# Kernel tuning notes

Hardware: AMD Instinct MI355X
Metric: run time of the kernel (lower is better)

Reference implementation:

```python
import jax, jax.numpy as jnp
import numpy as np

N_VARS = 28
HID = 64
BATCH = 32768
BN_EPS = 1e-5


def _lin_init(key, fan_in, shape):
    bound = 1.0 / np.sqrt(fan_in)
    return jax.random.uniform(key, shape, minval=-bound, maxval=bound, dtype=jnp.float32)


def setup_inputs() -> dict:
    key = jax.random.key(0)
    ks = jax.random.split(key, 8)
    n, h = N_VARS, HID
    X = jax.random.normal(ks[0], (BATCH, n), dtype=jnp.float32)
    W_logits = jax.random.uniform(ks[1], (n, n), minval=-0.01, maxval=0.01, dtype=jnp.float32)
    # per-mechanism (grouped) weights, stacked on leading mechanism axis n
    W1 = _lin_init(ks[2], n, (n, h, n)); b1 = _lin_init(ks[3], n, (n, h))
    W2 = _lin_init(ks[4], h, (n, h, h)); b2 = _lin_init(ks[5], h, (n, h))
    W3 = _lin_init(ks[6], h, (n, 1, h)); b3 = _lin_init(ks[7], h, (n, 1))
    gamma1 = jnp.ones((n, h)); beta1 = jnp.zeros((n, h))
    gamma2 = jnp.ones((n, h)); beta2 = jnp.zeros((n, h))
    return {"X": X, "W_logits": W_logits,
            "W1": W1, "b1": b1, "gamma1": gamma1, "beta1": beta1,
            "W2": W2, "b2": b2, "gamma2": gamma2, "beta2": beta2,
            "W3": W3, "b3": b3}


def _bn(x, gamma, beta):
    # x: [n, B, h]; batch stats over B (training-mode BatchNorm1d, biased var)
    m = x.mean(axis=1, keepdims=True)
    v = ((x - m) ** 2).mean(axis=1, keepdims=True)
    return gamma[:, None, :] * (x - m) * jax.lax.rsqrt(v + BN_EPS) + beta[:, None, :]


def reference(X, W_logits, W1, b1, gamma1, beta1, W2, b2, gamma2, beta2, W3, b3):
    n = W_logits.shape[0]
    # adjacency: sigmoid with zeroed diagonal
    W = jax.nn.sigmoid(W_logits) * (1.0 - jnp.eye(n, dtype=W_logits.dtype))
    # fuse the parent mask into the first layer's weights: one grouped GEMM
    # instead of n_vars separate masked matmuls
    W1_eff = W1 * W[:, None, :]                               # [n, h, n]
    h1 = jnp.einsum('bd,nhd->nbh', X, W1_eff) + b1[:, None, :]  # [n, B, h]
    a1 = jax.nn.gelu(_bn(h1, gamma1, beta1), approximate=False)
    h2 = jnp.einsum('nbh,ngh->nbg', a1, W2) + b2[:, None, :]
    a2 = jax.nn.gelu(_bn(h2, gamma2, beta2), approximate=False)
    out = jnp.einsum('nbh,noh->nbo', a2, W3) + b3[:, None, :]   # [n, B, 1]
    X_hat = out[:, :, 0].T                                     # [B, n]
    return (X_hat, W)
```

## Files before the change

### kernel.cpp

```cpp
#include <hip/hip_runtime.h>
#include <hip/hip_bf16.h>
#include <math.h>

typedef float  f4 __attribute__((ext_vector_type(4)));
typedef short  s8 __attribute__((ext_vector_type(8)));
typedef short  s4 __attribute__((ext_vector_type(4)));

#define NV 28
#define NB 32768
#define BN_EPS 1e-5f
#define NSLOT 434

#define SUM2_OFF   0
#define SSQ2_OFF   1792
#define BIAS1_OFF  3584
#define REDU_OFF   5376
#define PART_OFF   5824
#define BF_BASE_F  116992
#define W2B_OFF_S  57344
#define XBF_OFF_S  172032
#define H2_BYTE_OFF 2909184ull
#define H2_BYTES    117440512ull

__device__ __forceinline__ float gelu_f(float x) {
    float x2 = x * x;
    float z  = x * __builtin_fmaf(x2, -0.10294324f, -2.3022082f);
    float t  = __builtin_amdgcn_exp2f(z);
    return x * __builtin_amdgcn_rcpf(1.0f + t);
}
__device__ __forceinline__ unsigned short f2bf(float x) {
    unsigned u = __builtin_bit_cast(unsigned, x);
    return (unsigned short)((u + 0x7fffu + ((u >> 16) & 1u)) >> 16);
}
__device__ __forceinline__ float bf2f(short s) {
    return __builtin_bit_cast(float, ((int)(unsigned short)s) << 16);
}
__device__ __forceinline__ float row16_sum(float v) {
    int x;
    x = __builtin_amdgcn_update_dpp(0, __builtin_bit_cast(int, v), 0xB1, 0xF, 0xF, true);
    v += __builtin_bit_cast(float, x);
    x = __builtin_amdgcn_update_dpp(0, __builtin_bit_cast(int, v), 0x4E, 0xF, 0xF, true);
    v += __builtin_bit_cast(float, x);
    x = __builtin_amdgcn_update_dpp(0, __builtin_bit_cast(int, v), 0x124, 0xF, 0xF, true);
    v += __builtin_bit_cast(float, x);
    x = __builtin_amdgcn_update_dpp(0, __builtin_bit_cast(int, v), 0x128, 0xF, 0xF, true);
    v += __builtin_bit_cast(float, x);
    return v;
}
__device__ __forceinline__ float quad4_sum(float v) {
    int x;
    x = __builtin_amdgcn_update_dpp(0, __builtin_bit_cast(int, v), 0xB1, 0xF, 0xF, true);
    v += __builtin_bit_cast(float, x);
    x = __builtin_amdgcn_update_dpp(0, __builtin_bit_cast(int, v), 0x4E, 0xF, 0xF, true);
    v += __builtin_bit_cast(float, x);
    return v;
}

__global__ __launch_bounds__(256) void k_xstats(const float* __restrict__ X,
                                                float* __restrict__ ws) {
    __shared__ float sx[128 * 28];
    const int tid = threadIdx.x;
    const int rowbase = blockIdx.x * 128;
    {
        const f4* src = (const f4*)(X + (size_t)rowbase * 28);
        f4* dst = (f4*)sx;
        for (int i = tid; i < 128 * 28 / 4; i += 256) dst[i] = src[i];
    }
    __syncthreads();
    int* xb = (int*)((short*)(ws + BF_BASE_F) + XBF_OFF_S);
    for (int j = tid; j < 128 * 16; j += 256) {
        int row = j >> 4, cc = j & 15;
        float lo = (2 * cc     < 28) ? sx[row * 28 + 2 * cc]     : 0.0f;
        float hi = (2 * cc + 1 < 28) ? sx[row * 28 + 2 * cc + 1] : 0.0f;
        xb[(size_t)(rowbase + row) * 16 + cc] = (int)f2bf(lo) | ((int)f2bf(hi) << 16);
    }
    for (int s = tid; s < NSLOT; s += 256) {
        float a = 0.0f;
        if (s < 28) {
            for (int r = 0; r < 128; ++r) a += sx[r * 28 + s];
        } else {
            int p = s - 28, d = 0, rem = 28;
            while (p >= rem) { p -= rem; ++d; --rem; }
            int e = d + p;
            for (int r = 0; r < 128; ++r)
                a = __builtin_fmaf(sx[r * 28 + d], sx[r * 28 + e], a);
        }
        ws[PART_OFF + blockIdx.x * NSLOT + s] = a;
    }
}

__global__ __launch_bounds__(256) void k_reduce(float* __restrict__ ws) {
    int s = blockIdx.x * 256 + threadIdx.x;
    if (s < NSLOT) {
        float a = 0.0f;
#pragma unroll 16
        for (int p = 0; p < 256; ++p) a += ws[PART_OFF + p * NSLOT + s];
        ws[REDU_OFF + s] = a;
    }
}

__global__ __launch_bounds__(256) void k_fold1(const float* __restrict__ Wlog,
                                               const float* __restrict__ W1,
                                               const float* __restrict__ g1,
                                               const float* __restrict__ be1,
                                               const float* __restrict__ W2,
                                               float* __restrict__ ws,
                                               float* __restrict__ out_w) {
    __shared__ float mu[28], wrow[28];
    __shared__ float C[784];
    __shared__ float w1e_s[64 * 28];
    const int n = blockIdx.x, t = threadIdx.x;

    if (t < 28) {
        mu[t] = ws[REDU_OFF + t] * (1.0f / 32768.0f);
        float w = 1.0f / (1.0f + expf(-Wlog[n * 28 + t]));
        if (t == n) w = 0.0f;
        wrow[t] = w;
        out_w[n * 28 + t] = w;
    }
    if (t < 64) {
        ws[SUM2_OFF + n * 64 + t] = 0.0f;
        ws[SSQ2_OFF + n * 64 + t] = 0.0f;
    }
    __syncthreads();
    for (int i = t; i < 784; i += 256) {
        int d = i / 28, e = i % 28;
        int lo = d < e ? d : e, hi = d < e ? e : d;
        int idx = 28 + lo * 28 - (lo * (lo - 1)) / 2 + (hi - lo);
        C[i] = ws[REDU_OFF + idx] * (1.0f / 32768.0f) - mu[d] * mu[e];
    }
    for (int i = t; i < 1792; i += 256)
        w1e_s[i] = W1[(size_t)n * 1792 + i] * wrow[i % 28];
    __syncthreads();

    const int h = t >> 2, j = t & 3;
    const float* we = &w1e_s[h * 28];
    float var_p = 0.0f, dot_p = 0.0f;
#pragma unroll
    for (int k = 0; k < 7; ++k) {
        int d = 7 * j + k;
        float inner = 0.0f;
#pragma unroll
        for (int e = 0; e < 28; ++e) inner = __builtin_fmaf(C[d * 28 + e], we[e], inner);
        float wd = we[d];
        var_p = __builtin_fmaf(inner, wd, var_p);
        dot_p = __builtin_fmaf(wd, mu[d], dot_p);
    }
    float var  = quad4_sum(var_p);
    float dotm = quad4_sum(dot_p);
    float scale = g1[n * 64 + h] * rsqrtf(fmaxf(var, 0.0f) + BN_EPS);
    if (j == 0)
        ws[BIAS1_OFF + n * 64 + h] = be1[n * 64 + h] - dotm * scale;

    short* bfbase = (short*)(ws + BF_BASE_F);
    {
        short* w1f = bfbase + (size_t)(n * 64 + h) * 32;
        s8 pk;
#pragma unroll
        for (int k = 0; k < 8; ++k) {
            int d = 8 * j + k;
            pk[k] = (short)f2bf(d < 28 ? we[d] * scale : 0.0f);
        }
        *(s8*)&w1f[8 * j] = pk;
    }
    {
        const float* w2src = W2 + (size_t)n * 4096 + t * 16;
        short* w2d = bfbase + W2B_OFF_S + (size_t)n * 4096 + t * 16;
        s8 a, b;
#pragma unroll
        for (int k = 0; k < 8; ++k) a[k] = (short)f2bf(w2src[k]);
#pragma unroll
        for (int k = 0; k < 8; ++k) b[k] = (short)f2bf(w2src[8 + k]);
        *(s8*)&w2d[0] = a;
        *(s8*)&w2d[8] = b;
    }
}

template <bool STORE>
__global__ __launch_bounds__(256, 4) void k_pass1(float* __restrict__ ws,
                                                  short* __restrict__ h2buf) {
    __shared__ __align__(16) short sW1[64 * 40];
    __shared__ __align__(16) short sW2[64 * 72];
    __shared__ __align__(16) short sA1[8 * 16 * 72];
    __shared__ float sP1[4][64], sP2[4][64];

    const int n = blockIdx.x >> 7;
    const int blk = blockIdx.x & 127;
    const int tid = threadIdx.x;
    const int wave = tid >> 6;
    const int lane = tid & 63;
    const int m = lane & 15;
    const int q = lane >> 4;

    const short* bfbase = (const short*)(ws + BF_BASE_F);
    const short* w1g = bfbase + (size_t)n * 64 * 32;
    const short* w2g = bfbase + W2B_OFF_S + (size_t)n * 64 * 64;
    const short* xbf = bfbase + XBF_OFF_S;
    {
        int r = tid >> 2, c = tid & 3;
        *(s8*)&sW1[r * 40 + c * 8] = *(const s8*)&w1g[r * 32 + c * 8];
#pragma unroll
        for (int k = 0; k < 2; ++k) {
            int i2 = tid + k * 256;
            int r2 = i2 >> 3, c2 = i2 & 7;
            *(s8*)&sW2[r2 * 72 + c2 * 8] = *(const s8*)&w2g[r2 * 64 + c2 * 8];
        }
    }
    __syncthreads();

    const float* bias1 = ws + BIAS1_OFF + n * 64;
    short* myA1a = &sA1[(wave * 2 + 0) * 16 * 72];
    short* myA1b = &sA1[(wave * 2 + 1) * 16 * 72];
    float s1[16], s2v[16];
#pragma unroll
    for (int i = 0; i < 16; ++i) { s1[i] = 0.0f; s2v[i] = 0.0f; }

#pragma unroll
    for (int it = 0; it < 2; ++it) {
        const int row0 = blk * 256 + it * 128 + wave * 32;
        s8 xfa = *(const s8*)&xbf[(size_t)(row0 + m) * 32 + 8 * q];
        s8 xfb = *(const s8*)&xbf[(size_t)(row0 + 16 + m) * 32 + 8 * q];

        f4 acc1a[4], acc1b[4];
#pragma unroll
        for (int t = 0; t < 4; ++t) {
            s8 wf = *(const s8*)&sW1[(16 * t + m) * 40 + q * 8];
            acc1a[t] = __builtin_amdgcn_mfma_f32_16x16x32_bf16(wf, xfa, (f4){0.f, 0.f, 0.f, 0.f}, 0, 0, 0);
            acc1b[t] = __builtin_amdgcn_mfma_f32_16x16x32_bf16(wf, xfb, (f4){0.f, 0.f, 0.f, 0.f}, 0, 0, 0);
        }
#pragma unroll
        for (int t = 0; t < 4; ++t) {
            f4 bv = *(const f4*)&bias1[16 * t + 4 * q];
            s4 pa, pb;
#pragma unroll
            for (int r = 0; r < 4; ++r) {
                pa[r] = (short)f2bf(gelu_f(acc1a[t][r] + bv[r]));
                pb[r] = (short)f2bf(gelu_f(acc1b[t][r] + bv[r]));
            }
            *(s4*)&myA1a[m * 72 + 16 * t + 4 * q] = pa;
            *(s4*)&myA1b[m * 72 + 16 * t + 4 * q] = pb;
        }
        s8 af0a = *(const s8*)&myA1a[m * 72 + 8 * q];
        s8 af1a = *(const s8*)&myA1a[m * 72 + 32 + 8 * q];
        s8 af0b = *(const s8*)&myA1b[m * 72 + 8 * q];
        s8 af1b = *(const s8*)&myA1b[m * 72 + 32 + 8 * q];
        short* hpA = STORE ? (h2buf + ((size_t)n * NB + row0 + m) * 64) : nullptr;
        short* hpB = STORE ? (h2buf + ((size_t)n * NB + row0 + 16 + m) * 64) : nullptr;
#pragma unroll
        for (int u = 0; u < 4; ++u) {
            s8 w0 = *(const s8*)&sW2[(16 * u + m) * 72 + 8 * q];
            s8 w1 = *(const s8*)&sW2[(16 * u + m) * 72 + 32 + 8 * q];
            f4 aa = (f4){0.f, 0.f, 0.f, 0.f};
            f4 ab = (f4){0.f, 0.f, 0.f, 0.f};
            aa = __builtin_amdgcn_mfma_f32_16x16x32_bf16(w0, af0a, aa, 0, 0, 0);
            ab = __builtin_amdgcn_mfma_f32_16x16x32_bf16(w0, af0b, ab, 0, 0, 0);
            aa = __builtin_amdgcn_mfma_f32_16x16x32_bf16(w1, af1a, aa, 0, 0, 0);
            ab = __builtin_amdgcn_mfma_f32_16x16x32_bf16(w1, af1b, ab, 0, 0, 0);
            if (STORE) {
                s4 ha, hb;
#pragma unroll
                for (int r = 0; r < 4; ++r) { ha[r] = (short)f2bf(aa[r]); hb[r] = (short)f2bf(ab[r]); }
                *(s4*)&hpA[16 * u + 4 * q] = ha;
                *(s4*)&hpB[16 * u + 4 * q] = hb;
            }
#pragma unroll
            for (int r = 0; r < 4; ++r) {
                s1[u * 4 + r]  += aa[r] + ab[r];
                s2v[u * 4 + r] = __builtin_fmaf(aa[r], aa[r], s2v[u * 4 + r]);
                s2v[u * 4 + r] = __builtin_fmaf(ab[r], ab[r], s2v[u * 4 + r]);
            }
        }
    }
#pragma unroll
    for (int u = 0; u < 4; ++u) {
#pragma unroll
        for (int r = 0; r < 4; ++r) {
            float t1 = row16_sum(s1[u * 4 + r]);
            float t2 = row16_sum(s2v[u * 4 + r]);
            if (m == 0) {
                sP1[wave][16 * u + 4 * q + r] = t1;
                sP2[wave][16 * u + 4 * q + r] = t2;
            }
        }
    }
    __syncthreads();
    if (tid < 64) {
        float a = sP1[0][tid] + sP1[1][tid] + sP1[2][tid] + sP1[3][tid];
        float b = sP2[0][tid] + sP2[1][tid] + sP2[2][tid] + sP2[3][tid];
        atomicAdd(&ws[SUM2_OFF + n * 64 + tid], a);
        atomicAdd(&ws[SSQ2_OFF + n * 64 + tid], b);
    }
}

__global__ __launch_bounds__(256) void k_pass2s(const float* __restrict__ g2,
                                                const float* __restrict__ be2,
                                                const float* __restrict__ W3,
                                                const float* __restrict__ b3,
                                                const float* __restrict__ ws,
                                                const short* __restrict__ h2buf,
                                                float* __restrict__ out) {
    __shared__ float sSc[64], sSh[64], sW3v[64];
    const int n = blockIdx.x >> 7;
    const int row = ((blockIdx.x & 127) << 8) + threadIdx.x;
    if (threadIdx.x < 64) {
        int g = threadIdx.x;
        float mean = ws[SUM2_OFF + n * 64 + g] * (1.0f / 32768.0f);
        float var  = ws[SSQ2_OFF + n * 64 + g] * (1.0f / 32768.0f) - mean * mean;
        float sc = g2[n * 64 + g] * rsqrtf(fmaxf(var, 0.0f) + BN_EPS);
        sSc[g]  = sc;
        sSh[g]  = be2[n * 64 + g] - mean * sc;
        sW3v[g] = W3[n * 64 + g];
    }
    __syncthreads();
    const short* hp = h2buf + ((size_t)n * NB + row) * 64;
    float p = 0.0f;
#pragma unroll
    for (int c = 0; c < 8; ++c) {
        s8 hv = *(const s8*)&hp[c * 8];
#pragma unroll
        for (int k = 0; k < 8; ++k) {
            int g = c * 8 + k;
            float v = bf2f(hv[k]);
            p = __builtin_fmaf(gelu_f(__builtin_fmaf(v, sSc[g], sSh[g])), sW3v[g], p);
        }
    }
    out[(size_t)row * 28 + n] = p + b3[n];
}

__global__ __launch_bounds__(256, 4) void k_pass2r(const float* __restrict__ g2,
                                                   const float* __restrict__ be2,
                                                   const float* __restrict__ W3,
                                                   const float* __restrict__ b3,
                                                   float* __restrict__ ws,
                                                   float* __restrict__ out) {
    __shared__ __align__(16) short sW1[64 * 40];
    __shared__ __align__(16) short sW2[64 * 72];
    __shared__ __align__(16) short sA1[8 * 16 * 72];
    __shared__ float sSc[64], sSh[64], sW3v[64];

    const int n = blockIdx.x >> 7;
    const int blk = blockIdx.x & 127;
    const int tid = threadIdx.x;
    const int wave = tid >> 6;
    const int lane = tid & 63;
    const int m = lane & 15;
    const int q = lane >> 4;

    const short* bfbase = (const short*)(ws + BF_BASE_F);
    const short* w1g = bfbase + (size_t)n * 64 * 32;
    const short* w2g = bfbase + W2B_OFF_S + (size_t)n * 64 * 64;
    const short* xbf = bfbase + XBF_OFF_S;
    {
        int r = tid >> 2, c = tid & 3;
        *(s8*)&sW1[r * 40 + c * 8] = *(const s8*)&w1g[r * 32 + c * 8];
#pragma unroll
        for (int k = 0; k < 2; ++k) {
            int i2 = tid + k * 256;
            int r2 = i2 >> 3, c2 = i2 & 7;
            *(s8*)&sW2[r2 * 72 + c2 * 8] = *(const s8*)&w2g[r2 * 64 + c2 * 8];
        }
        if (tid < 64) {
            float mean = ws[SUM2_OFF + n * 64 + tid] * (1.0f / 32768.0f);
            float var  = ws[SSQ2_OFF + n * 64 + tid] * (1.0f / 32768.0f) - mean * mean;
            float sc = g2[n * 64 + tid] * rsqrtf(fmaxf(var, 0.0f) + BN_EPS);
            sSc[tid]  = sc;
            sSh[tid]  = be2[n * 64 + tid] - mean * sc;
            sW3v[tid] = W3[n * 64 + tid];
        }
    }
    __syncthreads();

    const float* bias1 = ws + BIAS1_OFF + n * 64;
    const float b3n = b3[n];
    short* myA1a = &sA1[(wave * 2 + 0) * 16 * 72];
    short* myA1b = &sA1[(wave * 2 + 1) * 16 * 72];

#pragma unroll
    for (int it = 0; it < 2; ++it) {
        const int row0 = blk * 256 + it * 128 + wave * 32;
        s8 xfa = *(const s8*)&xbf[(size_t)(row0 + m) * 32 + 8 * q];
        s8 xfb = *(const s8*)&xbf[(size_t)(row0 + 16 + m) * 32 + 8 * q];

        f4 acc1a[4], acc1b[4];
#pragma unroll
        for (int t = 0; t < 4; ++t) {
            s8 wf = *(const s8*)&sW1[(16 * t + m) * 40 + q * 8];
            acc1a[t] = __builtin_amdgcn_mfma_f32_16x16x32_bf16(wf, xfa, (f4){0.f, 0.f, 0.f, 0.f}, 0, 0, 0);
            acc1b[t] = __builtin_amdgcn_mfma_f32_16x16x32_bf16(wf, xfb, (f4){0.f, 0.f, 0.f, 0.f}, 0, 0, 0);
        }
#pragma unroll
        for (int t = 0; t < 4; ++t) {
            f4 bv = *(const f4*)&bias1[16 * t + 4 * q];
            s4 pa, pb;
#pragma unroll
            for (int r = 0; r < 4; ++r) {
                pa[r] = (short)f2bf(gelu_f(acc1a[t][r] + bv[r]));
                pb[r] = (short)f2bf(gelu_f(acc1b[t][r] + bv[r]));
            }
            *(s4*)&myA1a[m * 72 + 16 * t + 4 * q] = pa;
            *(s4*)&myA1b[m * 72 + 16 * t + 4 * q] = pb;
        }
        s8 af0a = *(const s8*)&myA1a[m * 72 + 8 * q];
        s8 af1a = *(const s8*)&myA1a[m * 72 + 32 + 8 * q];
        s8 af0b = *(const s8*)&myA1b[m * 72 + 8 * q];
        s8 af1b = *(const s8*)&myA1b[m * 72 + 32 + 8 * q];
        float pa = 0.0f, pb = 0.0f;
#pragma unroll
        for (int u = 0; u < 4; ++u) {
            s8 w0 = *(const s8*)&sW2[(16 * u + m) * 72 + 8 * q];
            s8 w1 = *(const s8*)&sW2[(16 * u + m) * 72 + 32 + 8 * q];
            f4 aa = (f4){0.f, 0.f, 0.f, 0.f};
            f4 ab = (f4){0.f, 0.f, 0.f, 0.f};
            aa = __builtin_amdgcn_mfma_f32_16x16x32_bf16(w0, af0a, aa, 0, 0, 0);
            ab = __builtin_amdgcn_mfma_f32_16x16x32_bf16(w0, af0b, ab, 0, 0, 0);
            aa = __builtin_amdgcn_mfma_f32_16x16x32_bf16(w1, af1a, aa, 0, 0, 0);
            ab = __builtin_amdgcn_mfma_f32_16x16x32_bf16(w1, af1b, ab, 0, 0, 0);
            f4 scv = *(const f4*)&sSc[16 * u + 4 * q];
            f4 shv = *(const f4*)&sSh[16 * u + 4 * q];
            f4 w3v = *(const f4*)&sW3v[16 * u + 4 * q];
#pragma unroll
            for (int r = 0; r < 4; ++r) {
                float va = __builtin_fmaf(aa[r], scv[r], shv[r]);
                float vb = __builtin_fmaf(ab[r], scv[r], shv[r]);
                pa = __builtin_fmaf(gelu_f(va), w3v[r], pa);
                pb = __builtin_fmaf(gelu_f(vb), w3v[r], pb);
            }
        }
        pa += __shfl_xor(pa, 16);  pa += __shfl_xor(pa, 32);
        pb += __shfl_xor(pb, 16);  pb += __shfl_xor(pb, 32);
        if (q == 0) {
            out[(size_t)(row0 + m) * 28 + n]      = pa + b3n;
            out[(size_t)(row0 + 16 + m) * 28 + n] = pb + b3n;
        }
    }
}

extern "C" void kernel_launch(void* const* d_in, const int* in_sizes, int n_in,
                              void* d_out, int out_size, void* d_ws, size_t ws_size,
                              hipStream_t stream) {
    const float* X   = (const float*)d_in[0];
    const float* Wl  = (const float*)d_in[1];
    const float* W1  = (const float*)d_in[2];
    const float* g1  = (const float*)d_in[4];
    const float* be1 = (const float*)d_in[5];
    const float* W2  = (const float*)d_in[6];
    const float* g2  = (const float*)d_in[8];
    const float* be2 = (const float*)d_in[9];
    const float* W3  = (const float*)d_in[10];
    const float* b3  = (const float*)d_in[11];
    float* out = (float*)d_out;
    float* ws  = (float*)d_ws;
    short* h2buf = (short*)((char*)d_ws + H2_BYTE_OFF);
    const bool store_h2 = ws_size >= H2_BYTE_OFF + H2_BYTES;

    k_xstats<<<dim3(256), dim3(256), 0, stream>>>(X, ws);
    k_reduce<<<dim3(2), dim3(256), 0, stream>>>(ws);
    k_fold1<<<dim3(28), dim3(256), 0, stream>>>(Wl, W1, g1, be1, W2, ws, out + 917504);
    if (store_h2) {
        k_pass1<true><<<dim3(28 * 128), dim3(256), 0, stream>>>(ws, h2buf);
        k_pass2s<<<dim3(28 * 128), dim3(256), 0, stream>>>(g2, be2, W3, b3, ws, h2buf, out);
    } else {
        k_pass1<false><<<dim3(28 * 128), dim3(256), 0, stream>>>(ws, nullptr);
        k_pass2r<<<dim3(28 * 128), dim3(256), 0, stream>>>(g2, be2, W3, b3, ws, out);
    }
}
```

Before: 187.4 us.

## Fold partial-stat reduction into k_fold1, per-wave atomics, raise pass1 occupancy

Removes the separate k_reduce launch by having each k_fold1 block redundantly sum the 256 partial statistic slots into shared memory. k_pass1 drops its cross-wave shared-memory reduction and barrier in favour of direct per-wave atomicAdds, hoists the bias loads out of the loop, and raises the launch bound to 5 blocks per CU. k_pass2s splits its dot-product accumulator in two to shorten the dependency chain. The cost is redundant reduction work in 28 blocks and four times as many atomics contending on the same addresses.

```diff
diff --git a/kernel.cpp b/kernel.cpp
--- a/kernel.cpp
+++ b/kernel.cpp
@@ -14,12 +14,11 @@
 #define SUM2_OFF   0
 #define SSQ2_OFF   1792
 #define BIAS1_OFF  3584
-#define REDU_OFF   5376
-#define PART_OFF   5824
-#define BF_BASE_F  116992
+#define PART_OFF   9472
+#define BF_BASE_F  120640
 #define W2B_OFF_S  57344
 #define XBF_OFF_S  172032
-#define H2_BYTE_OFF 2909184ull
+#define H2_BYTE_OFF 2924544ull
 #define H2_BYTES    117440512ull
 
 __device__ __forceinline__ float gelu_f(float x) {
@@ -89,16 +88,6 @@
     }
 }
 
-__global__ __launch_bounds__(256) void k_reduce(float* __restrict__ ws) {
-    int s = blockIdx.x * 256 + threadIdx.x;
-    if (s < NSLOT) {
-        float a = 0.0f;
-#pragma unroll 16
-        for (int p = 0; p < 256; ++p) a += ws[PART_OFF + p * NSLOT + s];
-        ws[REDU_OFF + s] = a;
-    }
-}
-
 __global__ __launch_bounds__(256) void k_fold1(const float* __restrict__ Wlog,
                                                const float* __restrict__ W1,
                                                const float* __restrict__ g1,
@@ -106,28 +95,37 @@
                                                const float* __restrict__ W2,
                                                float* __restrict__ ws,
                                                float* __restrict__ out_w) {
+    __shared__ float sstat[NSLOT];
     __shared__ float mu[28], wrow[28];
     __shared__ float C[784];
     __shared__ float w1e_s[64 * 28];
     const int n = blockIdx.x, t = threadIdx.x;
 
+    for (int s = t; s < NSLOT; s += 256) {
+        float a = 0.0f;
+#pragma unroll 16
+        for (int p = 0; p < 256; ++p) a += ws[PART_OFF + p * NSLOT + s];
+        sstat[s] = a;
+    }
+    if (t < 64) {
+        ws[SUM2_OFF + n * 64 + t] = 0.0f;
+        ws[SSQ2_OFF + n * 64 + t] = 0.0f;
+    }
+    __syncthreads();
+
     if (t < 28) {
-        mu[t] = ws[REDU_OFF + t] * (1.0f / 32768.0f);
+        mu[t] = sstat[t] * (1.0f / 32768.0f);
         float w = 1.0f / (1.0f + expf(-Wlog[n * 28 + t]));
         if (t == n) w = 0.0f;
         wrow[t] = w;
         out_w[n * 28 + t] = w;
     }
-    if (t < 64) {
-        ws[SUM2_OFF + n * 64 + t] = 0.0f;
-        ws[SSQ2_OFF + n * 64 + t] = 0.0f;
-    }
     __syncthreads();
     for (int i = t; i < 784; i += 256) {
         int d = i / 28, e = i % 28;
         int lo = d < e ? d : e, hi = d < e ? e : d;
         int idx = 28 + lo * 28 - (lo * (lo - 1)) / 2 + (hi - lo);
-        C[i] = ws[REDU_OFF + idx] * (1.0f / 32768.0f) - mu[d] * mu[e];
+        C[i] = sstat[idx] * (1.0f / 32768.0f) - mu[d] * mu[e];
     }
     for (int i = t; i < 1792; i += 256)
         w1e_s[i] = W1[(size_t)n * 1792 + i] * wrow[i % 28];
@@ -177,12 +175,11 @@
 }
 
 template <bool STORE>
-__global__ __launch_bounds__(256, 4) void k_pass1(float* __restrict__ ws,
+__global__ __launch_bounds__(256, 5) void k_pass1(float* __restrict__ ws,
                                                   short* __restrict__ h2buf) {
     __shared__ __align__(16) short sW1[64 * 40];
     __shared__ __align__(16) short sW2[64 * 72];
     __shared__ __align__(16) short sA1[8 * 16 * 72];
-    __shared__ float sP1[4][64], sP2[4][64];
 
     const int n = blockIdx.x >> 7;
     const int blk = blockIdx.x & 127;
@@ -209,6 +206,10 @@
     __syncthreads();
 
     const float* bias1 = ws + BIAS1_OFF + n * 64;
+    f4 biasv[4];
+#pragma unroll
+    for (int t = 0; t < 4; ++t) biasv[t] = *(const f4*)&bias1[16 * t + 4 * q];
+
     short* myA1a = &sA1[(wave * 2 + 0) * 16 * 72];
     short* myA1b = &sA1[(wave * 2 + 1) * 16 * 72];
     float s1[16], s2v[16];
@@ -230,12 +231,11 @@
         }
 #pragma unroll
         for (int t = 0; t < 4; ++t) {
-            f4 bv = *(const f4*)&bias1[16 * t + 4 * q];
             s4 pa, pb;
 #pragma unroll
             for (int r = 0; r < 4; ++r) {
-                pa[r] = (short)f2bf(gelu_f(acc1a[t][r] + bv[r]));
-                pb[r] = (short)f2bf(gelu_f(acc1b[t][r] + bv[r]));
+                pa[r] = (short)f2bf(gelu_f(acc1a[t][r] + biasv[t][r]));
+                pb[r] = (short)f2bf(gelu_f(acc1b[t][r] + biasv[t][r]));
             }
             *(s4*)&myA1a[m * 72 + 16 * t + 4 * q] = pa;
             *(s4*)&myA1b[m * 72 + 16 * t + 4 * q] = pb;
@@ -278,17 +278,10 @@
             float t1 = row16_sum(s1[u * 4 + r]);
             float t2 = row16_sum(s2v[u * 4 + r]);
             if (m == 0) {
-                sP1[wave][16 * u + 4 * q + r] = t1;
-                sP2[wave][16 * u + 4 * q + r] = t2;
-            }
-        }
-    }
-    __syncthreads();
-    if (tid < 64) {
-        float a = sP1[0][tid] + sP1[1][tid] + sP1[2][tid] + sP1[3][tid];
-        float b = sP2[0][tid] + sP2[1][tid] + sP2[2][tid] + sP2[3][tid];
-        atomicAdd(&ws[SUM2_OFF + n * 64 + tid], a);
-        atomicAdd(&ws[SSQ2_OFF + n * 64 + tid], b);
+                atomicAdd(&ws[SUM2_OFF + n * 64 + 16 * u + 4 * q + r], t1);
+                atomicAdd(&ws[SSQ2_OFF + n * 64 + 16 * u + 4 * q + r], t2);
+            }
+        }
     }
 }
 
@@ -313,18 +306,19 @@
     }
     __syncthreads();
     const short* hp = h2buf + ((size_t)n * NB + row) * 64;
-    float p = 0.0f;
+    float p0 = 0.0f, p1 = 0.0f;
 #pragma unroll
     for (int c = 0; c < 8; ++c) {
         s8 hv = *(const s8*)&hp[c * 8];
 #pragma unroll
         for (int k = 0; k < 8; ++k) {
             int g = c * 8 + k;
-            float v = bf2f(hv[k]);
-            p = __builtin_fmaf(gelu_f(__builtin_fmaf(v, sSc[g], sSh[g])), sW3v[g], p);
-        }
-    }
-    out[(size_t)row * 28 + n] = p + b3[n];
+            float v = __builtin_fmaf(bf2f(hv[k]), sSc[g], sSh[g]);
+            if (k & 1) p1 = __builtin_fmaf(gelu_f(v), sW3v[g], p1);
+            else       p0 = __builtin_fmaf(gelu_f(v), sW3v[g], p0);
+        }
+    }
+    out[(size_t)row * 28 + n] = p0 + p1 + b3[n];
 }
 
 __global__ __launch_bounds__(256, 4) void k_pass2r(const float* __restrict__ g2,
@@ -454,7 +448,6 @@
     const bool store_h2 = ws_size >= H2_BYTE_OFF + H2_BYTES;
 
     k_xstats<<<dim3(256), dim3(256), 0, stream>>>(X, ws);
-    k_reduce<<<dim3(2), dim3(256), 0, stream>>>(ws);
     k_fold1<<<dim3(28), dim3(256), 0, stream>>>(Wl, W1, g1, be1, W2, ws, out + 917504);
     if (store_h2) {
         k_pass1<true><<<dim3(28 * 128), dim3(256), 0, stream>>>(ws, h2buf);
```

Result: slower. 332.2 us (+77.3%).
